# Optimization experiments

Hardware: AMD Instinct MI355X
Metric: run time of the kernel (lower is better)

Reference implementation:

```python
import jax, jax.numpy as jnp
import numpy as np
from jax import lax

B, C, H, W = 16, 256, 56, 56
GROUPS = 4
K = 3
DILATIONS = (1, 3, 5)
EPS = 1e-5


@jax.custom_vjp
def bin_act(x):
    return jnp.sign(x)

def _bin_act_fwd(x):
    return jnp.sign(x), x

def _bin_act_bwd(x, g):
    grad = jnp.where((x >= -1.0) & (x <= 0.0), 2.0 + 2.0 * x, 0.0) \
         + jnp.where((x > 0.0) & (x <= 1.0), 2.0 - 2.0 * x, 0.0)
    return (grad * g,)

bin_act.defvjp(_bin_act_fwd, _bin_act_bwd)


def _bin_weight(wi):
    # per-output-channel scaling from raw |w|, centered sign, clip-STE
    scale = lax.stop_gradient(jnp.mean(jnp.abs(wi), axis=(1, 2, 3), keepdims=True))
    wc = wi - jnp.mean(wi, axis=(1, 2, 3), keepdims=True)
    clipped = jnp.clip(wc, -1.0, 1.0)
    return lax.stop_gradient(scale * jnp.sign(wc) - clipped) + clipped


def setup_inputs() -> dict:
    key = jax.random.key(0)
    ks = jax.random.split(key, 3)
    x = jax.random.normal(ks[0], (B, C, H, W), dtype=jnp.float32)
    # 3 branches of grouped conv weights: (3, C_out, C_in/groups, K, K)
    w = jax.random.normal(ks[1], (3, C, C // GROUPS, K, K), dtype=jnp.float32) * 0.05
    cb = jax.random.normal(ks[2], (3, C), dtype=jnp.float32) * 0.01
    return {
        "x": x,
        "bias": jnp.zeros((1, C, 1, 1), jnp.float32),   # LearnableBias
        "w": w,
        "cb": cb,                                        # conv biases
        "move1": jnp.zeros((3, C), jnp.float32),
        "alpha": jnp.full((3, C), 0.25, jnp.float32),    # PReLU slopes
        "move2": jnp.zeros((3, C), jnp.float32),
        "gamma": jnp.ones((C,), jnp.float32),            # LayerNorm weight
        "beta": jnp.zeros((C,), jnp.float32),            # LayerNorm bias
    }


def reference(x, bias, w, cb, move1, alpha, move2, gamma, beta):
    xb = x + bias
    xq = bin_act(xb)  # binarized activations, shared across branches
    out = jnp.zeros_like(x)
    for i, d in enumerate(DILATIONS):
        wq = _bin_weight(w[i])
        y = lax.conv_general_dilated(
            xq, wq,
            window_strides=(1, 1),
            padding=[(d, d), (d, d)],  # 'same' for k=3 with dilation d
            rhs_dilation=(d, d),
            dimension_numbers=("NCHW", "OIHW", "NCHW"),
            feature_group_count=GROUPS,
        )
        y = y + cb[i][None, :, None, None]
        # RPReLU: shift, channel-wise PReLU, shift
        y = y - move1[i][None, :, None, None]
        y = jnp.where(y >= 0, y, alpha[i][None, :, None, None] * y)
        y = y + move2[i][None, :, None, None]
        out = out + y
    # LayerNorm over channel dim (equivalent to NHWC last-dim LN)
    mean = jnp.mean(out, axis=1, keepdims=True)
    var = jnp.var(out, axis=1, keepdims=True)
    out = (out - mean) * lax.rsqrt(var + EPS)
    out = out * gamma[None, :, None, None] + beta[None, :, None, None]
    return out
```

## Files before the change

### kernel.cpp

```cpp
#include <hip/hip_runtime.h>
#include <stdint.h>

static constexpr int Bc = 16, Cc = 256, Hc = 56, Wc = 56, Gc = 4, CGc = 64;
static constexpr int HWc = Hc * Wc;
static constexpr float EPSc = 1e-5f;

__global__ __launch_bounds__(64) void k_prep(
    const float* __restrict__ w, const float* __restrict__ x,
    const float* __restrict__ bias, uint64_t* __restrict__ wbits,
    float* __restrict__ scales, uint64_t* __restrict__ abits) {
  if (blockIdx.x < 3 * Cc) {
    const int io = blockIdx.x;
    const int i = io >> 8, o = io & 255;
    const int lane = threadIdx.x;
    const float* wp = w + (size_t)io * 576 + lane * 9;
    float v[9];
    float ssum = 0.f, sabs = 0.f;
#pragma unroll
    for (int t = 0; t < 9; ++t) {
      v[t] = wp[t];
      ssum += v[t];
      sabs += fabsf(v[t]);
    }
#pragma unroll
    for (int off = 32; off > 0; off >>= 1) {
      ssum += __shfl_down(ssum, off);
      sabs += __shfl_down(sabs, off);
    }
    const float mean = __shfl(ssum, 0) * (1.f / 576.f);
    const float scale = __shfl(sabs, 0) * (1.f / 576.f);
#pragma unroll
    for (int t = 0; t < 9; ++t) {
      unsigned long long m = __ballot(v[t] > mean);
      if (lane == 0) wbits[(i * 9 + t) * Cc + o] = m;
    }
    if (lane == 0) scales[io] = scale;
  } else {
    const int bid = blockIdx.x - 3 * Cc;
    const int h = bid % Hc;
    const int bg = bid / Hc;
    const int g = bg & 3;
    const int ww = threadIdx.x;
    if (ww >= Wc) return;
    const float* xp = x + (((size_t)(bg >> 2) * Cc + g * CGc) * Hc + h) * Wc + ww;
    const float* bp = bias + g * CGc;
    uint64_t word = 0;
#pragma unroll
    for (int ci = 0; ci < CGc; ++ci) {
      const float s = xp[(size_t)ci * HWc] + bp[ci];
      word |= (uint64_t)(s > 0.f) << ci;
    }
    abits[(size_t)bid * Wc + ww] = word;
  }
}

template <int D>
struct Branch {
  uint64_t wgt[9];
  const uint64_t *r0, *r1, *r2;
  int BL, BM, BR;
  float sc, cbm1, al;

  __device__ __forceinline__ void init(const uint64_t* __restrict__ wb,
                                       const uint64_t* arow,
                                       const uint64_t* zrow, int h,
                                       float sc_, float cbm1_, float al_) {
    sc = sc_; cbm1 = cbm1_; al = al_;
    int z[9];
#pragma unroll
    for (int k = 0; k < 9; ++k) {
      wgt[k] = wb[k * Cc];
      z[k] = 64 - 2 * (int)__popcll(wgt[k]);
    }
    const bool v0 = (h - D >= 0), v2 = (h + D < Hc);
    r0 = v0 ? (arow + (5 - D) * Wc) : zrow;
    r1 = arow + 5 * Wc;
    r2 = v2 ? (arow + (5 + D) * Wc) : zrow;
    const int Z0 = (v0 ? 0 : z[0]) + (v2 ? 0 : z[6]);
    const int Z1 = (v0 ? 0 : z[1]) + (v2 ? 0 : z[7]);
    const int Z2 = (v0 ? 0 : z[2]) + (v2 ? 0 : z[8]);
    BM = 576 - Z0 - Z1 - Z2;
    BL = 384 - Z1 - Z2;
    BR = 384 - Z0 - Z1;
  }

  __device__ __forceinline__ float eval(int w) const {
    int P = 0;
#pragma unroll
    for (int kh = 0; kh < 3; ++kh) {
      const uint64_t* rp = (kh == 0) ? r0 : (kh == 1 ? r1 : r2);
#pragma unroll
      for (int kw = 0; kw < 3; ++kw) {
        const int col = w + D * (kw - 1);
        if (col < 0 || col >= Wc) continue;
        P += (int)__popcll(wgt[kh * 3 + kw] ^ rp[col]);
      }
    }
    const int B = (w < D) ? BL : ((w >= Wc - D) ? BR : BM);
    const float y0 = fmaf(sc, (float)(B - 2 * P), cbm1);
    return (y0 >= 0.f) ? y0 : al * y0;
  }
};

static constexpr int TS = 57;
static constexpr int ZOFF = Gc * 11 * Wc;

__global__ __launch_bounds__(256) void k_conv_ln(
    const uint64_t* __restrict__ abits, const uint64_t* __restrict__ wbits,
    const float* __restrict__ scales, const float* __restrict__ cb,
    const float* __restrict__ mv1, const float* __restrict__ al,
    const float* __restrict__ mv2, const float* __restrict__ gamma,
    const float* __restrict__ beta, float* __restrict__ out) {
  __shared__ uint64_t a_lds[Gc * 11 * Wc + Wc];
  __shared__ float out_tile[Cc * TS];
  __shared__ float redu[4][Wc], redq[4][Wc];
  __shared__ float mstat[Wc], rstat[Wc];

  const int bid = blockIdx.x;
  const int b = bid / Hc, h = bid % Hc;
  const int t = threadIdx.x;
  const int g = t >> 6;

  for (int idx = t; idx < Gc * 11 * Wc; idx += 256) {
    const int w = idx % Wc;
    const int rem = idx / Wc;
    const int r = rem % 11;
    const int gg = rem / 11;
    const int row = h + r - 5;
    uint64_t v = 0;
    if (row >= 0 && row < Hc)
      v = abits[(((size_t)b * Gc + gg) * Hc + row) * Wc + w];
    a_lds[idx] = v;
  }
  if (t < Wc) a_lds[ZOFF + t] = 0;
  __syncthreads();

  const uint64_t* arow = a_lds + g * 11 * Wc;
  const uint64_t* zrow = a_lds + ZOFF;
  Branch<1> b0; Branch<3> b1; Branch<5> b2;
  b0.init(wbits + 0 * 9 * Cc + t, arow, zrow, h, scales[0 * Cc + t],
          cb[0 * Cc + t] - mv1[0 * Cc + t], al[0 * Cc + t]);
  b1.init(wbits + 1 * 9 * Cc + t, arow, zrow, h, scales[1 * Cc + t],
          cb[1 * Cc + t] - mv1[1 * Cc + t], al[1 * Cc + t]);
  b2.init(wbits + 2 * 9 * Cc + t, arow, zrow, h, scales[2 * Cc + t],
          cb[2 * Cc + t] - mv1[2 * Cc + t], al[2 * Cc + t]);
  const float m2sum = mv2[0 * Cc + t] + mv2[1 * Cc + t] + mv2[2 * Cc + t];

#pragma unroll
  for (int w = 0; w < Wc; ++w) {
    const float outv = m2sum + b0.eval(w) + b1.eval(w) + b2.eval(w);
    out_tile[t * TS + w] = outv;
  }
  __syncthreads();

  if (t < 4 * Wc) {
    const int w = t % Wc;
    const int cq = t / Wc;
    float s = 0.f, sq = 0.f;
#pragma unroll 4
    for (int c = cq * 64; c < cq * 64 + 64; ++c) {
      const float v = out_tile[c * TS + w];
      s += v;
      sq = fmaf(v, v, sq);
    }
    redu[cq][w] = s;
    redq[cq][w] = sq;
  }
  __syncthreads();
  if (t < Wc) {
    const float s = redu[0][t] + redu[1][t] + redu[2][t] + redu[3][t];
    const float sq = redq[0][t] + redq[1][t] + redq[2][t] + redq[3][t];
    const float mean = s * (1.f / 256.f);
    const float var = sq * (1.f / 256.f) - mean * mean;
    mstat[t] = mean;
    rstat[t] = rsqrtf(var + EPSc);
  }
  __syncthreads();

  float* base = out + ((size_t)b * Cc * Hc + h) * Wc;
  for (int idx = t; idx < Cc * Wc; idx += 256) {
    const int c = idx / Wc;
    const int w = idx - c * Wc;
    const float v = out_tile[c * TS + w];
    base[(size_t)c * HWc + w] = (v - mstat[w]) * rstat[w] * gamma[c] + beta[c];
  }
}

extern "C" void kernel_launch(void* const* d_in, const int* in_sizes, int n_in,
                              void* d_out, int out_size, void* d_ws, size_t ws_size,
                              hipStream_t stream) {
  const float* x     = (const float*)d_in[0];
  const float* bias  = (const float*)d_in[1];
  const float* w     = (const float*)d_in[2];
  const float* cb    = (const float*)d_in[3];
  const float* mv1   = (const float*)d_in[4];
  const float* al    = (const float*)d_in[5];
  const float* mv2   = (const float*)d_in[6];
  const float* gamma = (const float*)d_in[7];
  const float* beta  = (const float*)d_in[8];
  float* out = (float*)d_out;

  uint8_t* ws = (uint8_t*)d_ws;
  uint64_t* abits = (uint64_t*)ws;
  uint64_t* wbits = (uint64_t*)(ws + (size_t)200704 * 8);
  float* scales   = (float*)(ws + (size_t)200704 * 8 + 6912 * 8);

  hipLaunchKernelGGL(k_prep, dim3(3 * Cc + Bc * Gc * Hc), dim3(64), 0, stream,
                     w, x, bias, wbits, scales, abits);
  hipLaunchKernelGGL(k_conv_ln, dim3(Bc * Hc), dim3(256), 0, stream,
                     abits, wbits, scales, cb, mv1, al, mv2, gamma, beta, out);
}
```

Baseline: 192.2 us.

## Restructure activation packing, read bit rows from global, stage outputs in half

The prep kernel now packs activation bits per (batch,row) block. It reads x with coalesced float4 loads, transposes through a shared byte buffer and gathers the bytes into 64-bit words. Weight binarisation now packs four output channels per block. The conv kernel drops the shared activation staging, reads bit rows straight from global/L2 into register windows of 14 columns, and stores the pre-LayerNorm tile as fp16 to cut LDS use and allow 4 blocks per CU. The fp16 tile lowers the precision of the LayerNorm inputs and outputs, and the register-window loads raise register pressure.

```diff
diff --git a/kernel.cpp b/kernel.cpp
--- a/kernel.cpp
+++ b/kernel.cpp
@@ -1,26 +1,32 @@
 #include <hip/hip_runtime.h>
+#include <hip/hip_fp16.h>
 #include <stdint.h>
 
 static constexpr int Bc = 16, Cc = 256, Hc = 56, Wc = 56, Gc = 4, CGc = 64;
 static constexpr int HWc = Hc * Wc;
 static constexpr float EPSc = 1e-5f;
 
-__global__ __launch_bounds__(64) void k_prep(
+
+static constexpr int SBS = 260;
+
+__global__ __launch_bounds__(256) void k_prep(
     const float* __restrict__ w, const float* __restrict__ x,
     const float* __restrict__ bias, uint64_t* __restrict__ wbits,
-    float* __restrict__ scales, uint64_t* __restrict__ abits) {
-  if (blockIdx.x < 3 * Cc) {
-    const int io = blockIdx.x;
+    float* __restrict__ scales, uint64_t* __restrict__ abits,
+    uint32_t* __restrict__ zero_area) {
+  const int t = threadIdx.x;
+  if (blockIdx.x < 192) {
+    const int io = blockIdx.x * 4 + (t >> 6);
     const int i = io >> 8, o = io & 255;
-    const int lane = threadIdx.x;
+    const int lane = t & 63;
     const float* wp = w + (size_t)io * 576 + lane * 9;
     float v[9];
     float ssum = 0.f, sabs = 0.f;
 #pragma unroll
-    for (int t = 0; t < 9; ++t) {
-      v[t] = wp[t];
-      ssum += v[t];
-      sabs += fabsf(v[t]);
+    for (int k = 0; k < 9; ++k) {
+      v[k] = wp[k];
+      ssum += v[k];
+      sabs += fabsf(v[k]);
     }
 #pragma unroll
     for (int off = 32; off > 0; off >>= 1) {
@@ -30,27 +36,42 @@
     const float mean = __shfl(ssum, 0) * (1.f / 576.f);
     const float scale = __shfl(sabs, 0) * (1.f / 576.f);
 #pragma unroll
-    for (int t = 0; t < 9; ++t) {
-      unsigned long long m = __ballot(v[t] > mean);
-      if (lane == 0) wbits[(i * 9 + t) * Cc + o] = m;
+    for (int k = 0; k < 9; ++k) {
+      unsigned long long m = __ballot(v[k] > mean);
+      if (lane == 0) wbits[(i * 9 + k) * Cc + o] = m;
     }
     if (lane == 0) scales[io] = scale;
+  } else if (blockIdx.x == 192) {
+    zero_area[t] = 0;
   } else {
-    const int bid = blockIdx.x - 3 * Cc;
-    const int h = bid % Hc;
-    const int bg = bid / Hc;
-    const int g = bg & 3;
-    const int ww = threadIdx.x;
-    if (ww >= Wc) return;
-    const float* xp = x + (((size_t)(bg >> 2) * Cc + g * CGc) * Hc + h) * Wc + ww;
-    const float* bp = bias + g * CGc;
-    uint64_t word = 0;
-#pragma unroll
-    for (int ci = 0; ci < CGc; ++ci) {
-      const float s = xp[(size_t)ci * HWc] + bp[ci];
-      word |= (uint64_t)(s > 0.f) << ci;
-    }
-    abits[(size_t)bid * Wc + ww] = word;
+    __shared__ uint8_t sb[Wc * SBS];
+    const int bid = blockIdx.x - 193;
+    const int b = bid / Hc, h = bid % Hc;
+    const float* xb = x + ((size_t)b * Cc) * HWc + h * Wc;
+#pragma unroll
+    for (int k = 0; k < 14; ++k) {
+      const int idx = k * 256 + t;
+      const int c = idx / 14, q = idx - c * 14;
+      const float4 v = *(const float4*)(xb + (size_t)c * HWc + q * 4);
+      const float bc = bias[c];
+      sb[(q * 4 + 0) * SBS + c] = (v.x + bc > 0.f);
+      sb[(q * 4 + 1) * SBS + c] = (v.y + bc > 0.f);
+      sb[(q * 4 + 2) * SBS + c] = (v.z + bc > 0.f);
+      sb[(q * 4 + 3) * SBS + c] = (v.w + bc > 0.f);
+    }
+    __syncthreads();
+    if (t < Gc * Wc) {
+      const int g = t / Wc, ww = t - g * Wc;
+      const uint32_t* p = (const uint32_t*)(sb + ww * SBS + g * 64);
+      uint64_t word = 0;
+#pragma unroll
+      for (int dw = 0; dw < 16; ++dw) {
+        const uint32_t d = p[dw];
+        const uint32_t nib = (d | (d >> 7) | (d >> 14) | (d >> 21)) & 0xF;
+        word |= (uint64_t)nib << (4 * dw);
+      }
+      abits[(((size_t)b * Gc + g) * Hc + h) * Wc + ww] = word;
+    }
   }
 }
 
@@ -62,7 +83,7 @@
   float sc, cbm1, al;
 
   __device__ __forceinline__ void init(const uint64_t* __restrict__ wb,
-                                       const uint64_t* arow,
+                                       const uint64_t* rowbase,
                                        const uint64_t* zrow, int h,
                                        float sc_, float cbm1_, float al_) {
     sc = sc_; cbm1 = cbm1_; al = al_;
@@ -70,12 +91,12 @@
 #pragma unroll
     for (int k = 0; k < 9; ++k) {
       wgt[k] = wb[k * Cc];
-      z[k] = 64 - 2 * (int)__popcll(wgt[k]);
+      z[k] = 64 - 2 * (int)__builtin_popcountll(wgt[k]);
     }
     const bool v0 = (h - D >= 0), v2 = (h + D < Hc);
-    r0 = v0 ? (arow + (5 - D) * Wc) : zrow;
-    r1 = arow + 5 * Wc;
-    r2 = v2 ? (arow + (5 + D) * Wc) : zrow;
+    r0 = v0 ? (rowbase + (size_t)(h - D) * Wc) : zrow;
+    r1 = rowbase + (size_t)h * Wc;
+    r2 = v2 ? (rowbase + (size_t)(h + D) * Wc) : zrow;
     const int Z0 = (v0 ? 0 : z[0]) + (v2 ? 0 : z[6]);
     const int Z1 = (v0 ? 0 : z[1]) + (v2 ? 0 : z[7]);
     const int Z2 = (v0 ? 0 : z[2]) + (v2 ? 0 : z[8]);
@@ -84,87 +105,97 @@
     BR = 384 - Z0 - Z1;
   }
 
-  __device__ __forceinline__ float eval(int w) const {
-    int P = 0;
+  __device__ __forceinline__ void accum(int c0, int acc[14]) const {
 #pragma unroll
     for (int kh = 0; kh < 3; ++kh) {
       const uint64_t* rp = (kh == 0) ? r0 : (kh == 1 ? r1 : r2);
-#pragma unroll
-      for (int kw = 0; kw < 3; ++kw) {
-        const int col = w + D * (kw - 1);
-        if (col < 0 || col >= Wc) continue;
-        P += (int)__popcll(wgt[kh * 3 + kw] ^ rp[col]);
+      uint64_t sa[14 + 2 * D];
+#pragma unroll
+      for (int j = 0; j < 14 + 2 * D; ++j) sa[j] = rp[c0 - D + j];
+#pragma unroll
+      for (int ww = 0; ww < 14; ++ww) {
+#pragma unroll
+        for (int kw = 0; kw < 3; ++kw) {
+          const int col = c0 + ww + D * (kw - 1);
+          if (col < 0 || col >= Wc) continue;
+          acc[ww] += (int)__builtin_popcountll(wgt[kh * 3 + kw] ^ sa[ww + D * kw]);
+        }
       }
     }
-    const int B = (w < D) ? BL : ((w >= Wc - D) ? BR : BM);
-    const float y0 = fmaf(sc, (float)(B - 2 * P), cbm1);
-    return (y0 >= 0.f) ? y0 : al * y0;
+  }
+
+  __device__ __forceinline__ void epi(int c0, const int acc[14],
+                                      float outf[14]) const {
+#pragma unroll
+    for (int ww = 0; ww < 14; ++ww) {
+      const int wg = c0 + ww;
+      const int B = (wg < D) ? BL : ((wg >= Wc - D) ? BR : BM);
+      const float y0 = fmaf(sc, (float)(B - 2 * acc[ww]), cbm1);
+      outf[ww] += fmaxf(y0, 0.f) + al * fminf(y0, 0.f);
+    }
   }
 };
 
-static constexpr int TS = 57;
-static constexpr int ZOFF = Gc * 11 * Wc;
-
-__global__ __launch_bounds__(256) void k_conv_ln(
-    const uint64_t* __restrict__ abits, const uint64_t* __restrict__ wbits,
-    const float* __restrict__ scales, const float* __restrict__ cb,
-    const float* __restrict__ mv1, const float* __restrict__ al,
-    const float* __restrict__ mv2, const float* __restrict__ gamma,
-    const float* __restrict__ beta, float* __restrict__ out) {
-  __shared__ uint64_t a_lds[Gc * 11 * Wc + Wc];
-  __shared__ float out_tile[Cc * TS];
+static constexpr int TS2 = 58;
+
+__global__ __launch_bounds__(256, 4) void k_conv_ln(
+    const uint64_t* __restrict__ abits, const uint64_t* __restrict__ zrow,
+    const uint64_t* __restrict__ wbits, const float* __restrict__ scales,
+    const float* __restrict__ cb, const float* __restrict__ mv1,
+    const float* __restrict__ al, const float* __restrict__ mv2,
+    const float* __restrict__ gamma, const float* __restrict__ beta,
+    float* __restrict__ out) {
+  __shared__ __half out_tile[Cc * TS2];
   __shared__ float redu[4][Wc], redq[4][Wc];
   __shared__ float mstat[Wc], rstat[Wc];
 
   const int bid = blockIdx.x;
   const int b = bid / Hc, h = bid % Hc;
   const int t = threadIdx.x;
-  const int g = t >> 6;
-
-  for (int idx = t; idx < Gc * 11 * Wc; idx += 256) {
-    const int w = idx % Wc;
-    const int rem = idx / Wc;
-    const int r = rem % 11;
-    const int gg = rem / 11;
-    const int row = h + r - 5;
-    uint64_t v = 0;
-    if (row >= 0 && row < Hc)
-      v = abits[(((size_t)b * Gc + gg) * Hc + row) * Wc + w];
-    a_lds[idx] = v;
-  }
-  if (t < Wc) a_lds[ZOFF + t] = 0;
-  __syncthreads();
-
-  const uint64_t* arow = a_lds + g * 11 * Wc;
-  const uint64_t* zrow = a_lds + ZOFF;
+  const int gu = __builtin_amdgcn_readfirstlane(t >> 6);
+
+  const uint64_t* rowbase = abits + ((size_t)b * Gc + gu) * Hc * Wc;
+
   Branch<1> b0; Branch<3> b1; Branch<5> b2;
-  b0.init(wbits + 0 * 9 * Cc + t, arow, zrow, h, scales[0 * Cc + t],
+  b0.init(wbits + 0 * 9 * Cc + t, rowbase, zrow, h, scales[0 * Cc + t],
           cb[0 * Cc + t] - mv1[0 * Cc + t], al[0 * Cc + t]);
-  b1.init(wbits + 1 * 9 * Cc + t, arow, zrow, h, scales[1 * Cc + t],
+  b1.init(wbits + 1 * 9 * Cc + t, rowbase, zrow, h, scales[1 * Cc + t],
           cb[1 * Cc + t] - mv1[1 * Cc + t], al[1 * Cc + t]);
-  b2.init(wbits + 2 * 9 * Cc + t, arow, zrow, h, scales[2 * Cc + t],
+  b2.init(wbits + 2 * 9 * Cc + t, rowbase, zrow, h, scales[2 * Cc + t],
           cb[2 * Cc + t] - mv1[2 * Cc + t], al[2 * Cc + t]);
   const float m2sum = mv2[0 * Cc + t] + mv2[1 * Cc + t] + mv2[2 * Cc + t];
 
 #pragma unroll
-  for (int w = 0; w < Wc; ++w) {
-    const float outv = m2sum + b0.eval(w) + b1.eval(w) + b2.eval(w);
-    out_tile[t * TS + w] = outv;
+  for (int ch = 0; ch < 4; ++ch) {
+    const int c0 = ch * 14;
+    float outf[14];
+#pragma unroll
+    for (int ww = 0; ww < 14; ++ww) outf[ww] = m2sum;
+    { int acc[14] = {}; b0.accum(c0, acc); b0.epi(c0, acc, outf); }
+    { int acc[14] = {}; b1.accum(c0, acc); b1.epi(c0, acc, outf); }
+    { int acc[14] = {}; b2.accum(c0, acc); b2.epi(c0, acc, outf); }
+#pragma unroll
+    for (int ww = 0; ww < 14; ww += 2) {
+      __half2 hv;
+      hv.x = __float2half(outf[ww]);
+      hv.y = __float2half(outf[ww + 1]);
+      *(__half2*)&out_tile[t * TS2 + c0 + ww] = hv;
+    }
   }
   __syncthreads();
 
   if (t < 4 * Wc) {
-    const int w = t % Wc;
+    const int ww = t % Wc;
     const int cq = t / Wc;
     float s = 0.f, sq = 0.f;
 #pragma unroll 4
     for (int c = cq * 64; c < cq * 64 + 64; ++c) {
-      const float v = out_tile[c * TS + w];
+      const float v = __half2float(out_tile[c * TS2 + ww]);
       s += v;
       sq = fmaf(v, v, sq);
     }
-    redu[cq][w] = s;
-    redq[cq][w] = sq;
+    redu[cq][ww] = s;
+    redq[cq][ww] = sq;
   }
   __syncthreads();
   if (t < Wc) {
@@ -180,9 +211,9 @@
   float* base = out + ((size_t)b * Cc * Hc + h) * Wc;
   for (int idx = t; idx < Cc * Wc; idx += 256) {
     const int c = idx / Wc;
-    const int w = idx - c * Wc;
-    const float v = out_tile[c * TS + w];
-    base[(size_t)c * HWc + w] = (v - mstat[w]) * rstat[w] * gamma[c] + beta[c];
+    const int ww = idx - c * Wc;
+    const float v = __half2float(out_tile[c * TS2 + ww]);
+    base[(size_t)c * HWc + ww] = (v - mstat[ww]) * rstat[ww] * gamma[c] + beta[c];
   }
 }
 
@@ -201,12 +232,15 @@
   float* out = (float*)d_out;
 
   uint8_t* ws = (uint8_t*)d_ws;
-  uint64_t* abits = (uint64_t*)ws;
-  uint64_t* wbits = (uint64_t*)(ws + (size_t)200704 * 8);
-  float* scales   = (float*)(ws + (size_t)200704 * 8 + 6912 * 8);
-
-  hipLaunchKernelGGL(k_prep, dim3(3 * Cc + Bc * Gc * Hc), dim3(64), 0, stream,
-                     w, x, bias, wbits, scales, abits);
+  uint32_t* zero_area = (uint32_t*)ws;
+  const uint64_t* zrow = (const uint64_t*)(ws + 64);
+  uint64_t* abits = (uint64_t*)(ws + 1024);
+  uint64_t* wbits = (uint64_t*)(ws + 1024 + (size_t)200704 * 8);
+  float* scales   = (float*)(ws + 1024 + (size_t)200704 * 8 + 6912 * 8);
+
+  hipLaunchKernelGGL(k_prep, dim3(192 + 1 + Bc * Hc), dim3(256), 0, stream,
+                     w, x, bias, wbits, scales, abits, zero_area);
   hipLaunchKernelGGL(k_conv_ln, dim3(Bc * Hc), dim3(256), 0, stream,
-                     abits, wbits, scales, cb, mv1, al, mv2, gamma, beta, out);
+                     abits, zrow, wbits, scales, cb, mv1, al, mv2, gamma, beta,
+                     out);
 }
```

Measured after the change: 196.5 us. 1.02x slower.
